# Kernel tuning notes

Hardware: AMD Instinct MI355X
Metric: run time of the kernel (lower is better)

## Reference

```python
import jax, jax.numpy as jnp
import numpy as np

D_MODEL = 4096
NUM_EXPERTS = 64
TOP_K = 2


def setup_inputs() -> dict:
    key = jax.random.key(0)
    kx, kw, kb = jax.random.split(key, 3)
    x = jax.random.normal(kx, (4, 4096, D_MODEL), dtype=jnp.float32)
    # nn.Linear default init ~ U(-1/sqrt(fan_in), 1/sqrt(fan_in))
    bound = 1.0 / np.sqrt(D_MODEL)
    W = jax.random.uniform(kw, (D_MODEL, NUM_EXPERTS), minval=-bound, maxval=bound, dtype=jnp.float32)
    b = jax.random.uniform(kb, (NUM_EXPERTS,), minval=-bound, maxval=bound, dtype=jnp.float32)
    return {"x": x, "W": W, "b": b}


def reference(x, W, b):
    # gate: [B,S,D] @ [D,E] -> [B,S,E]
    logits = jnp.einsum('bsd,de->bse', x, W) + b
    probs = jax.nn.softmax(logits, axis=-1)
    topk_probs, topk_indices = jax.lax.top_k(probs, TOP_K)
    topk_probs = topk_probs / (jnp.sum(topk_probs, axis=-1, keepdims=True) + 1e-9)
    return probs, topk_probs, topk_indices
```

## Files before the change

### kernel.cpp

```cpp
#include <hip/hip_runtime.h>

#define D_MODEL 4096
#define NEXP    64
#define NTOK    16384
#define NKS     128

typedef _Float16 half8 __attribute__((ext_vector_type(8)));
typedef float    f32x4 __attribute__((ext_vector_type(4)));

__device__ __forceinline__ void split8(float4 a, float4 b, half8& hi, half8& lo) {
    auto h0 = __builtin_amdgcn_cvt_pkrtz(a.x, a.y);
    auto h1 = __builtin_amdgcn_cvt_pkrtz(a.z, a.w);
    auto h2 = __builtin_amdgcn_cvt_pkrtz(b.x, b.y);
    auto h3 = __builtin_amdgcn_cvt_pkrtz(b.z, b.w);
    hi[0] = static_cast<_Float16>(h0[0]); hi[1] = static_cast<_Float16>(h0[1]);
    hi[2] = static_cast<_Float16>(h1[0]); hi[3] = static_cast<_Float16>(h1[1]);
    hi[4] = static_cast<_Float16>(h2[0]); hi[5] = static_cast<_Float16>(h2[1]);
    hi[6] = static_cast<_Float16>(h3[0]); hi[7] = static_cast<_Float16>(h3[1]);
    float r0 = a.x - (float)h0[0], r1 = a.y - (float)h0[1];
    float r2 = a.z - (float)h1[0], r3 = a.w - (float)h1[1];
    float r4 = b.x - (float)h2[0], r5 = b.y - (float)h2[1];
    float r6 = b.z - (float)h3[0], r7 = b.w - (float)h3[1];
    auto l0 = __builtin_amdgcn_cvt_pkrtz(r0, r1);
    auto l1 = __builtin_amdgcn_cvt_pkrtz(r2, r3);
    auto l2 = __builtin_amdgcn_cvt_pkrtz(r4, r5);
    auto l3 = __builtin_amdgcn_cvt_pkrtz(r6, r7);
    lo[0] = static_cast<_Float16>(l0[0]); lo[1] = static_cast<_Float16>(l0[1]);
    lo[2] = static_cast<_Float16>(l1[0]); lo[3] = static_cast<_Float16>(l1[1]);
    lo[4] = static_cast<_Float16>(l2[0]); lo[5] = static_cast<_Float16>(l2[1]);
    lo[6] = static_cast<_Float16>(l3[0]); lo[7] = static_cast<_Float16>(l3[1]);
}

__global__ __launch_bounds__(256) void prep_w(const float* __restrict__ W,
                                              half8* __restrict__ ws) {
    const int gid  = blockIdx.x * 256 + threadIdx.x;
    const int lane = gid & 63;
    const int fp   = gid >> 6;
    const int t    = fp & 3;
    const int ks   = fp >> 2;
    const int e    = 16 * t + (lane & 15);
    const int k0   = ks * 32 + (lane >> 4) * 8;
    float4 a, b;
    a.x = W[(size_t)(k0 + 0) * NEXP + e];
    a.y = W[(size_t)(k0 + 1) * NEXP + e];
    a.z = W[(size_t)(k0 + 2) * NEXP + e];
    a.w = W[(size_t)(k0 + 3) * NEXP + e];
    b.x = W[(size_t)(k0 + 4) * NEXP + e];
    b.y = W[(size_t)(k0 + 5) * NEXP + e];
    b.z = W[(size_t)(k0 + 6) * NEXP + e];
    b.w = W[(size_t)(k0 + 7) * NEXP + e];
    half8 hi, lo;
    split8(a, b, hi, lo);
    ws[(size_t)(fp * 2 + 0) * 64 + lane] = hi;
    ws[(size_t)(fp * 2 + 1) * 64 + lane] = lo;
}

__global__ __launch_bounds__(256, 4) void router_mfma(
    const float* __restrict__ x, const int4* __restrict__ wf,
    const float* __restrict__ b, float* __restrict__ out)
{
    __shared__ float part[4][16][68];
    const int tid  = threadIdx.x;
    const int lane = tid & 63;
    const int wv   = tid >> 6;
    const int tok0 = blockIdx.x * 16;
    const int m    = lane & 15;
    const int q    = lane >> 4;
    const float* __restrict__ xrow =
        x + (size_t)(tok0 + m) * D_MODEL + wv * 1024 + q * 8;

    f32x4 acc[4] = {};

    float4 xaA, xbA, xaB, xbB;
    int4   wA[4][2], wB[4][2];

    auto ldj = [&](int j, float4& xa, float4& xb, int4 (&w)[4][2]) {
        const float* p = xrow + j * 32;
        xa = *(const float4*)p;
        xb = *(const float4*)(p + 4);
        const size_t base = (size_t)(wv * 32 + j) * 512 + lane;
#pragma unroll
        for (int t = 0; t < 4; t++) {
            w[t][0] = wf[base + t * 128];
            w[t][1] = wf[base + t * 128 + 64];
        }
    };
    auto cmp = [&](const float4& xa, const float4& xb, int4 (&w)[4][2]) {
        half8 ahi, alo;
        split8(xa, xb, ahi, alo);
#pragma unroll
        for (int t = 0; t < 4; t++) {
            half8 bhi = __builtin_bit_cast(half8, w[t][0]);
            half8 blo = __builtin_bit_cast(half8, w[t][1]);
            acc[t] = __builtin_amdgcn_mfma_f32_16x16x32_f16(ahi, bhi, acc[t], 0, 0, 0);
            acc[t] = __builtin_amdgcn_mfma_f32_16x16x32_f16(ahi, blo, acc[t], 0, 0, 0);
            acc[t] = __builtin_amdgcn_mfma_f32_16x16x32_f16(alo, bhi, acc[t], 0, 0, 0);
        }
    };

    ldj(0, xaA, xbA, wA);
#pragma unroll 1
    for (int j = 0; j < 32; j += 2) {
        ldj(j + 1, xaB, xbB, wB);
        cmp(xaA, xbA, wA);
        ldj((j + 2) & 31, xaA, xbA, wA);
        cmp(xaB, xbB, wB);
    }

#pragma unroll
    for (int t = 0; t < 4; t++)
#pragma unroll
        for (int r = 0; r < 4; r++)
            part[wv][q * 4 + r][t * 16 + m] = acc[t][r];
    __syncthreads();

    const float bias = b[lane];
    float* __restrict__ probs_out = out;
    float* __restrict__ top_out   = out + (size_t)NTOK * NEXP;
    float* __restrict__ idx_out   = top_out + (size_t)NTOK * 2;

#pragma unroll 1
    for (int r2 = 0; r2 < 4; r2++) {
        const int row   = wv * 4 + r2;
        const int token = tok0 + row;
        float logit = part[0][row][lane] + part[1][row][lane]
                    + part[2][row][lane] + part[3][row][lane] + bias;

        float mx = logit;
#pragma unroll
        for (int off = 32; off; off >>= 1) mx = fmaxf(mx, __shfl_xor(mx, off, 64));
        float ex = expf(logit - mx);
        float s = ex;
#pragma unroll
        for (int off = 32; off; off >>= 1) s += __shfl_xor(s, off, 64);
        float p = ex / s;
        probs_out[(size_t)token * NEXP + lane] = p;

        float v = p; int idx = lane;
#pragma unroll
        for (int off = 32; off; off >>= 1) {
            float ov = __shfl_xor(v, off, 64);
            int   oi = __shfl_xor(idx, off, 64);
            if (ov > v || (ov == v && oi < idx)) { v = ov; idx = oi; }
        }
        const float v1 = v; const int i1 = idx;
        v = (lane == i1) ? -1.0f : p; idx = lane;
#pragma unroll
        for (int off = 32; off; off >>= 1) {
            float ov = __shfl_xor(v, off, 64);
            int   oi = __shfl_xor(idx, off, 64);
            if (ov > v || (ov == v && oi < idx)) { v = ov; idx = oi; }
        }
        const float v2 = v; const int i2 = idx;

        if (lane == 0) {
            const float dnm = v1 + v2 + 1e-9f;
            top_out[(size_t)token * 2 + 0] = v1 / dnm;
            top_out[(size_t)token * 2 + 1] = v2 / dnm;
            idx_out[(size_t)token * 2 + 0] = (float)i1;
            idx_out[(size_t)token * 2 + 1] = (float)i2;
        }
    }
}

#define BK  128
#define BKP (BK + 4)
__device__ __forceinline__ float rl(float v, int l) {
    return __int_as_float(__builtin_amdgcn_readlane(__float_as_int(v), l));
}
__global__ __launch_bounds__(128) void router_fallback(
    const float* __restrict__ x, const float* __restrict__ W,
    const float* __restrict__ b, float* __restrict__ out)
{
    __shared__ float wt[NEXP * BKP];
    const int tid  = threadIdx.x;
    const int lane = tid & 63;
    const int wv   = __builtin_amdgcn_readfirstlane(tid >> 6);
    const int tok0 = blockIdx.x * 16 + wv * 8;
    const float* __restrict__ xw = x + (size_t)tok0 * D_MODEL;

    float2 xcur[8], xnxt[8];
#pragma unroll
    for (int t = 0; t < 8; t++)
        xcur[t] = *(const float2*)(xw + (size_t)t * D_MODEL + 2 * lane);
    float accm[8];
#pragma unroll
    for (int t = 0; t < 8; t++) accm[t] = 0.f;

    for (int c = 0; c < D_MODEL / BK; c++) {
        const int k0 = c * BK;
        if (c + 1 < D_MODEL / BK) {
#pragma unroll
            for (int t = 0; t < 8; t++)
                xnxt[t] = *(const float2*)(xw + (size_t)t * D_MODEL + (k0 + BK) + 2 * lane);
        }
#pragma unroll
        for (int i = 0; i < 16; i++) {
            int n  = i * 128 + tid;
            int dd = n >> 4;
            int e0 = (n & 15) * 4;
            float4 v = *(const float4*)(W + (size_t)(k0 + dd) * NEXP + e0);
            wt[(e0 + 0) * BKP + dd] = v.x;
            wt[(e0 + 1) * BKP + dd] = v.y;
            wt[(e0 + 2) * BKP + dd] = v.z;
            wt[(e0 + 3) * BKP + dd] = v.w;
        }
        __syncthreads();
        float acc[8];
#pragma unroll
        for (int t = 0; t < 8; t++) acc[t] = 0.f;
        const float* wl = &wt[lane * BKP];
#pragma unroll 4
        for (int kk = 0; kk < BK; kk += 4) {
            float4 w4 = *(const float4*)(wl + kk);
            const int l0 = kk >> 1;
#pragma unroll
            for (int t = 0; t < 8; t++) {
                float a = acc[t];
                a = fmaf(rl(xcur[t].x, l0    ), w4.x, a);
                a = fmaf(rl(xcur[t].y, l0    ), w4.y, a);
                a = fmaf(rl(xcur[t].x, l0 + 1), w4.z, a);
                a = fmaf(rl(xcur[t].y, l0 + 1), w4.w, a);
                acc[t] = a;
            }
        }
#pragma unroll
        for (int t = 0; t < 8; t++) accm[t] += acc[t];
        __syncthreads();
#pragma unroll
        for (int t = 0; t < 8; t++) xcur[t] = xnxt[t];
    }

    const float bias = b[lane];
    float* __restrict__ probs_out = out;
    float* __restrict__ top_out   = out + (size_t)NTOK * NEXP;
    float* __restrict__ idx_out   = top_out + (size_t)NTOK * 2;
#pragma unroll 1
    for (int t = 0; t < 8; t++) {
        const int token = tok0 + t;
        float logit = accm[t] + bias;
        float mx = logit;
#pragma unroll
        for (int off = 32; off; off >>= 1) mx = fmaxf(mx, __shfl_xor(mx, off, 64));
        float ex = expf(logit - mx);
        float s = ex;
#pragma unroll
        for (int off = 32; off; off >>= 1) s += __shfl_xor(s, off, 64);
        float p = ex / s;
        probs_out[(size_t)token * NEXP + lane] = p;
        float v = p; int idx = lane;
#pragma unroll
        for (int off = 32; off; off >>= 1) {
            float ov = __shfl_xor(v, off, 64);
            int   oi = __shfl_xor(idx, off, 64);
            if (ov > v || (ov == v && oi < idx)) { v = ov; idx = oi; }
        }
        const float v1 = v; const int i1 = idx;
        v = (lane == i1) ? -1.0f : p; idx = lane;
#pragma unroll
        for (int off = 32; off; off >>= 1) {
            float ov = __shfl_xor(v, off, 64);
            int   oi = __shfl_xor(idx, off, 64);
            if (ov > v || (ov == v && oi < idx)) { v = ov; idx = oi; }
        }
        const float v2 = v; const int i2 = idx;
        if (lane == 0) {
            const float dnm = v1 + v2 + 1e-9f;
            top_out[(size_t)token * 2 + 0] = v1 / dnm;
            top_out[(size_t)token * 2 + 1] = v2 / dnm;
            idx_out[(size_t)token * 2 + 0] = (float)i1;
            idx_out[(size_t)token * 2 + 1] = (float)i2;
        }
    }
}

extern "C" void kernel_launch(void* const* d_in, const int* in_sizes, int n_in,
                              void* d_out, int out_size, void* d_ws, size_t ws_size,
                              hipStream_t stream) {
    const float* x = (const float*)d_in[0];
    const float* W = (const float*)d_in[1];
    const float* b = (const float*)d_in[2];
    float* out = (float*)d_out;

    const size_t need = (size_t)NKS * 4 * 2 * 64 * 16;
    if (ws_size >= need) {
        prep_w<<<128, 256, 0, stream>>>(W, (half8*)d_ws);
        router_mfma<<<NTOK / 16, 256, 0, stream>>>(x, (const int4*)d_ws, b, out);
    } else {
        router_fallback<<<NTOK / 16, 128, 0, stream>>>(x, W, b, out);
    }
}
```

Measured before the change: 414.3 us.

## Stage x tiles into LDS via async global_load_lds with double buffering

Replaces direct register loads of x with asynchronous global-to-LDS DMA (global_load_lds) into a per-wave double-buffered 2x2048-float area. Compute reads x from LDS while the next tile streams in, synchronised with explicit vmcnt waits. The k-loop start is rotated per block and wave to spread DRAM/L2 access. LDS grows to 64KB per block, so launch bounds drop occupancy from 4 to 2 blocks per CU. The hand-written vmcnt counts are fragile against compiler reordering.

```diff
diff --git a/kernel.cpp b/kernel.cpp
--- a/kernel.cpp
+++ b/kernel.cpp
@@ -29,6 +29,13 @@
     lo[2] = static_cast<_Float16>(l1[0]); lo[3] = static_cast<_Float16>(l1[1]);
     lo[4] = static_cast<_Float16>(l2[0]); lo[5] = static_cast<_Float16>(l2[1]);
     lo[6] = static_cast<_Float16>(l3[0]); lo[7] = static_cast<_Float16>(l3[1]);
+}
+
+__device__ __forceinline__ void dma16(const float* g, float* l) {
+    __builtin_amdgcn_global_load_lds(
+        (const __attribute__((address_space(1))) unsigned int*)g,
+        (__attribute__((address_space(3))) unsigned int*)l,
+        16, 0, 0);
 }
 
 __global__ __launch_bounds__(256) void prep_w(const float* __restrict__ W,
@@ -55,11 +62,11 @@
     ws[(size_t)(fp * 2 + 1) * 64 + lane] = lo;
 }
 
-__global__ __launch_bounds__(256, 4) void router_mfma(
+__global__ __launch_bounds__(256, 2) void router_mfma(
     const float* __restrict__ x, const int4* __restrict__ wf,
     const float* __restrict__ b, float* __restrict__ out)
 {
-    __shared__ float part[4][16][68];
+    __shared__ float lds[4][4096];
     const int tid  = threadIdx.x;
     const int lane = tid & 63;
     const int wv   = tid >> 6;
@@ -68,50 +75,76 @@
     const int q    = lane >> 4;
     const float* __restrict__ xrow =
         x + (size_t)(tok0 + m) * D_MODEL + wv * 1024 + q * 8;
+    const int4* __restrict__ wq = wf + (size_t)wv * 32 * 512 + lane;
+    float* __restrict__ xs = lds[wv];
+
+    const int rot = (blockIdx.x ^ wv) & 7;
 
     f32x4 acc[4] = {};
-
-    float4 xaA, xbA, xaB, xbB;
-    int4   wA[4][2], wB[4][2];
-
-    auto ldj = [&](int j, float4& xa, float4& xb, int4 (&w)[4][2]) {
-        const float* p = xrow + j * 32;
-        xa = *(const float4*)p;
-        xb = *(const float4*)(p + 4);
-        const size_t base = (size_t)(wv * 32 + j) * 512 + lane;
+    int4  wba[4][2], wbb[4][2];
+
+    auto jof = [&](int bb) { return ((bb + rot) & 7) * 4; };
+
+    auto stage = [&](int bb, int buf) {
+        const int j0 = jof(bb);
+        float* dst = xs + buf * 2048;
+#pragma unroll
+        for (int s = 0; s < 4; s++) {
+            const float* src = xrow + (size_t)(j0 + s) * 32;
+            dma16(src,     dst + (s * 2 + 0) * 256);
+            dma16(src + 4, dst + (s * 2 + 1) * 256);
+        }
+    };
+    auto ldw = [&](int4 (&w)[4][2], int j) {
+        const int base = j * 512;
 #pragma unroll
         for (int t = 0; t < 4; t++) {
-            w[t][0] = wf[base + t * 128];
-            w[t][1] = wf[base + t * 128 + 64];
+            w[t][0] = wq[base + t * 128];
+            w[t][1] = wq[base + t * 128 + 64];
         }
     };
-    auto cmp = [&](const float4& xa, const float4& xb, int4 (&w)[4][2]) {
+    auto cmp = [&](int buf, int slot, int4 (&wb)[4][2]) {
+        const float* px = xs + buf * 2048 + slot * 512 + lane * 4;
+        float4 xa = *(const float4*)px;
+        float4 xb = *(const float4*)(px + 256);
         half8 ahi, alo;
         split8(xa, xb, ahi, alo);
 #pragma unroll
         for (int t = 0; t < 4; t++) {
-            half8 bhi = __builtin_bit_cast(half8, w[t][0]);
-            half8 blo = __builtin_bit_cast(half8, w[t][1]);
+            half8 bhi = __builtin_bit_cast(half8, wb[t][0]);
+            half8 blo = __builtin_bit_cast(half8, wb[t][1]);
             acc[t] = __builtin_amdgcn_mfma_f32_16x16x32_f16(ahi, bhi, acc[t], 0, 0, 0);
             acc[t] = __builtin_amdgcn_mfma_f32_16x16x32_f16(ahi, blo, acc[t], 0, 0, 0);
             acc[t] = __builtin_amdgcn_mfma_f32_16x16x32_f16(alo, bhi, acc[t], 0, 0, 0);
         }
     };
 
-    ldj(0, xaA, xbA, wA);
+    stage(0, 0);
+    ldw(wba, jof(0));
+
 #pragma unroll 1
-    for (int j = 0; j < 32; j += 2) {
-        ldj(j + 1, xaB, xbB, wB);
-        cmp(xaA, xbA, wA);
-        ldj((j + 2) & 31, xaA, xbA, wA);
-        cmp(xaB, xbB, wB);
+    for (int bb = 0; bb < 8; bb++) {
+        const int buf = bb & 1;
+        if (bb < 7) {
+            stage(bb + 1, buf ^ 1);
+            asm volatile("s_waitcnt vmcnt(8)" ::: "memory");
+        } else {
+            asm volatile("s_waitcnt vmcnt(0)" ::: "memory");
+        }
+        __builtin_amdgcn_sched_barrier(0);
+        const int j0 = jof(bb);
+        const int jn = jof((bb + 1) & 7);
+        ldw(wbb, j0 + 1); cmp(buf, 0, wba);
+        ldw(wba, j0 + 2); cmp(buf, 1, wbb);
+        ldw(wbb, j0 + 3); cmp(buf, 2, wba);
+        ldw(wba, jn);     cmp(buf, 3, wbb);
     }
 
 #pragma unroll
     for (int t = 0; t < 4; t++)
 #pragma unroll
         for (int r = 0; r < 4; r++)
-            part[wv][q * 4 + r][t * 16 + m] = acc[t][r];
+            xs[(q * 4 + r) * 68 + t * 16 + m] = acc[t][r];
     __syncthreads();
 
     const float bias = b[lane];
@@ -123,8 +156,8 @@
     for (int r2 = 0; r2 < 4; r2++) {
         const int row   = wv * 4 + r2;
         const int token = tok0 + row;
-        float logit = part[0][row][lane] + part[1][row][lane]
-                    + part[2][row][lane] + part[3][row][lane] + bias;
+        float logit = lds[0][row * 68 + lane] + lds[1][row * 68 + lane]
+                    + lds[2][row * 68 + lane] + lds[3][row * 68 + lane] + bias;
 
         float mx = logit;
 #pragma unroll
```

Result: faster. 392.0 us (-5.4%).

## Stage x tiles in LDS via async global_load_lds and split waves by expert

Applied to the files above, without the earlier changes.

Instead of each wave reading its own K-slice of x straight into registers and reducing partial sums across waves, the block now stages 16x256 tiles of x into double-buffered LDS with asynchronous global-to-LDS DMA. Every wave reads the full K range from LDS and computes a different 16-expert column tile, which removes the cross-wave reduction and cuts accumulator registers. The cost is two barriers per stage and a longer serial K loop per wave (128 k-steps instead of 32). The hand-placed vmcnt waits must track the outstanding loads exactly for correctness.

```diff
diff --git a/kernel.cpp b/kernel.cpp
--- a/kernel.cpp
+++ b/kernel.cpp
@@ -29,6 +29,13 @@
     lo[2] = static_cast<_Float16>(l1[0]); lo[3] = static_cast<_Float16>(l1[1]);
     lo[4] = static_cast<_Float16>(l2[0]); lo[5] = static_cast<_Float16>(l2[1]);
     lo[6] = static_cast<_Float16>(l3[0]); lo[7] = static_cast<_Float16>(l3[1]);
+}
+
+__device__ __forceinline__ void dma16(const float* g, float* l) {
+    __builtin_amdgcn_global_load_lds(
+        (const __attribute__((address_space(1))) unsigned int*)g,
+        (__attribute__((address_space(3))) unsigned int*)l,
+        16, 0, 0);
 }
 
 __global__ __launch_bounds__(256) void prep_w(const float* __restrict__ W,
@@ -59,59 +66,79 @@
     const float* __restrict__ x, const int4* __restrict__ wf,
     const float* __restrict__ b, float* __restrict__ out)
 {
-    __shared__ float part[4][16][68];
+    __shared__ float xs[2][16][260];
     const int tid  = threadIdx.x;
     const int lane = tid & 63;
     const int wv   = tid >> 6;
     const int tok0 = blockIdx.x * 16;
     const int m    = lane & 15;
     const int q    = lane >> 4;
-    const float* __restrict__ xrow =
-        x + (size_t)(tok0 + m) * D_MODEL + wv * 1024 + q * 8;
-
-    f32x4 acc[4] = {};
-
-    float4 xaA, xbA, xaB, xbB;
-    int4   wA[4][2], wB[4][2];
-
-    auto ldj = [&](int j, float4& xa, float4& xb, int4 (&w)[4][2]) {
-        const float* p = xrow + j * 32;
-        xa = *(const float4*)p;
-        xb = *(const float4*)(p + 4);
-        const size_t base = (size_t)(wv * 32 + j) * 512 + lane;
-#pragma unroll
-        for (int t = 0; t < 4; t++) {
-            w[t][0] = wf[base + t * 128];
-            w[t][1] = wf[base + t * 128 + 64];
-        }
+
+    const float* xsrc[4];
+#pragma unroll
+    for (int d = 0; d < 4; d++)
+        xsrc[d] = x + (size_t)(tok0 + wv * 4 + d) * D_MODEL + lane * 4;
+    const int4* __restrict__ wq = wf + lane;
+
+    f32x4 acc = {};
+    int4  wA[2], wB[2];
+
+    auto stage = [&](int w, int buf) {
+#pragma unroll
+        for (int d = 0; d < 4; d++)
+            dma16(xsrc[d] + w * 256, &xs[buf][wv * 4 + d][0]);
     };
-    auto cmp = [&](const float4& xa, const float4& xb, int4 (&w)[4][2]) {
+    auto ldw = [&](int4 (&W)[2], int ks) {
+        const int base = ks * 512 + wv * 128;
+        W[0] = wq[base];
+        W[1] = wq[base + 64];
+    };
+    auto cmp = [&](int buf, int s, int4 (&Wb)[2]) {
+        const float* px = &xs[buf][m][s * 32 + q * 8];
+        float4 xa = *(const float4*)px;
+        float4 xb = *(const float4*)(px + 4);
         half8 ahi, alo;
         split8(xa, xb, ahi, alo);
-#pragma unroll
-        for (int t = 0; t < 4; t++) {
-            half8 bhi = __builtin_bit_cast(half8, w[t][0]);
-            half8 blo = __builtin_bit_cast(half8, w[t][1]);
-            acc[t] = __builtin_amdgcn_mfma_f32_16x16x32_f16(ahi, bhi, acc[t], 0, 0, 0);
-            acc[t] = __builtin_amdgcn_mfma_f32_16x16x32_f16(ahi, blo, acc[t], 0, 0, 0);
-            acc[t] = __builtin_amdgcn_mfma_f32_16x16x32_f16(alo, bhi, acc[t], 0, 0, 0);
-        }
+        half8 bhi = __builtin_bit_cast(half8, Wb[0]);
+        half8 blo = __builtin_bit_cast(half8, Wb[1]);
+        acc = __builtin_amdgcn_mfma_f32_16x16x32_f16(ahi, bhi, acc, 0, 0, 0);
+        acc = __builtin_amdgcn_mfma_f32_16x16x32_f16(ahi, blo, acc, 0, 0, 0);
+        acc = __builtin_amdgcn_mfma_f32_16x16x32_f16(alo, bhi, acc, 0, 0, 0);
     };
 
-    ldj(0, xaA, xbA, wA);
+    ldw(wA, 0);
+    stage(0, 0);
+
 #pragma unroll 1
-    for (int j = 0; j < 32; j += 2) {
-        ldj(j + 1, xaB, xbB, wB);
-        cmp(xaA, xbA, wA);
-        ldj((j + 2) & 31, xaA, xbA, wA);
-        cmp(xaB, xbB, wB);
-    }
-
-#pragma unroll
-    for (int t = 0; t < 4; t++)
-#pragma unroll
-        for (int r = 0; r < 4; r++)
-            part[wv][q * 4 + r][t * 16 + m] = acc[t][r];
+    for (int w = 0; w < 16; w++) {
+        const int buf = w & 1;
+        if (w < 15) {
+            stage(w + 1, buf ^ 1);
+            asm volatile("s_waitcnt vmcnt(4)" ::: "memory");
+        } else {
+            asm volatile("s_waitcnt vmcnt(0)" ::: "memory");
+        }
+        __builtin_amdgcn_sched_barrier(0);
+        __builtin_amdgcn_s_barrier();
+        __builtin_amdgcn_sched_barrier(0);
+        const int ks0 = w * 8;
+#pragma unroll
+        for (int s = 0; s < 8; s += 2) {
+            ldw(wB, ks0 + s + 1);
+            cmp(buf, s, wA);
+            const int nk = (s == 6) ? ((w < 15) ? ks0 + 8 : 0) : ks0 + s + 2;
+            ldw(wA, nk);
+            cmp(buf, s + 1, wB);
+        }
+        __builtin_amdgcn_sched_barrier(0);
+        __builtin_amdgcn_s_barrier();
+        __builtin_amdgcn_sched_barrier(0);
+    }
+
+    float* part = &xs[0][0][0];
+#pragma unroll
+    for (int r = 0; r < 4; r++)
+        part[(q * 4 + r) * 68 + wv * 16 + m] = acc[r];
     __syncthreads();
 
     const float bias = b[lane];
@@ -123,8 +150,7 @@
     for (int r2 = 0; r2 < 4; r2++) {
         const int row   = wv * 4 + r2;
         const int token = tok0 + row;
-        float logit = part[0][row][lane] + part[1][row][lane]
-                    + part[2][row][lane] + part[3][row][lane] + bias;
+        float logit = part[row * 68 + lane] + bias;
 
         float mx = logit;
 #pragma unroll
```

After: 372.8 us. 1.11x faster.
